# Kernel tuning notes

Measured on AMD Instinct MI355X. Metric: run time of the kernel, lower is better.

Reference implementation:

```python
import jax, jax.numpy as jnp
import numpy as np

LN_EPS = 1e-5

def _ln(x, g):
    # LayerNorm with no bias, matching torch (population variance)
    m = x.mean(-1, keepdims=True)
    v = x.var(-1, keepdims=True)
    return (x - m) / jnp.sqrt(v + LN_EPS) * g


def setup_inputs() -> dict:
    key = jax.random.key(0)
    ks = jax.random.split(key, 10)
    B, S, D, L, V = 4, 4096, 256, 6, 32000
    std = 0.02  # nn.init.normal_(std=0.02)
    tokens = jax.random.randint(ks[0], (B, S), 0, V)
    wte = jax.random.normal(ks[1], (V, D), jnp.float32) * std
    wpe = jax.random.normal(ks[2], (S + 1, D), jnp.float32) * std  # context_size+1 table
    g_e = jnp.ones((D,), jnp.float32)
    g_p = jnp.ones((D,), jnp.float32)
    g_out = jnp.ones((D,), jnp.float32)
    ff_w1 = jax.random.normal(ks[3], (D, 4 * D), jnp.float32) * std
    ff_w2 = jax.random.normal(ks[4], (4 * D, D), jnp.float32) * std
    Wq = jax.random.normal(ks[5], (L, D, D), jnp.float32) * std
    Wk = jax.random.normal(ks[6], (L, D, D), jnp.float32) * std
    Wv = jax.random.normal(ks[7], (L, D, D), jnp.float32) * std
    return {"tokens": tokens, "wte": wte, "wpe": wpe, "g_e": g_e, "g_p": g_p,
            "g_out": g_out, "ff_w1": ff_w1, "ff_w2": ff_w2,
            "Wq": Wq, "Wk": Wk, "Wv": Wv}


def reference(tokens, wte, wpe, g_e, g_p, g_out, ff_w1, ff_w2, Wq, Wk, Wv):
    B, S = tokens.shape
    D = wte.shape[1]
    L = Wq.shape[0]
    # embeddings + pre-LN (dropout = identity at eval)
    e = _ln(wte[tokens], g_e)                 # [B,S,D] token stream
    p = _ln(wpe[:S], g_p)                     # [S,D]   positional stream (batch-invariant)
    x = e + p[None]                           # [B,S,D]
    # covariate FF on positional stream (use_ppe=True): p = p + W2 @ gelu(W1 @ p)
    p = p + jax.nn.gelu(p @ ff_w1, approximate=False) @ ff_w2
    causal = jnp.tril(jnp.ones((S, S), bool))
    inv_sqrt_d = D ** -0.5
    for l in range(L):
        # use_ppe: Q=K from positional stream (batch-invariant), V from token embeds
        q = p @ Wq[l]                          # [S,D]
        k = p @ Wk[l]                          # [S,D]
        v = jnp.einsum('bsd,de->bse', e, Wv[l])  # [B,S,D]
        s = (q @ k.T) * inv_sqrt_d             # [S,S], shared across batch
        s = jnp.where(causal, s, -jnp.inf)
        a = jax.nn.softmax(s, axis=-1)
        x = x + jnp.einsum('st,btd->bsd', a, v)
    # targets=None path: last position only
    x = x[:, -1:, :]                           # [B,1,D]
    x = _ln(x, g_out)                          # use_ln_out
    logits = x @ _ln(wte, g_e).T               # tied output head through ln_e
    return logits                              # [B,1,V]
```

## Files before the change

kernel.cpp:

```cpp
#include <hip/hip_runtime.h>
#include <hip/hip_bf16.h>

#define LN_EPS 1e-5f

typedef __attribute__((ext_vector_type(8))) short s8v;
typedef __attribute__((ext_vector_type(4))) float f32x4;

__device__ __forceinline__ float wred_sum(float v) {
#pragma unroll
  for (int o = 32; o > 0; o >>= 1) v += __shfl_xor(v, o, 64);
  return v;
}
__device__ __forceinline__ float wred_max(float v) {
#pragma unroll
  for (int o = 32; o > 0; o >>= 1) v = fmaxf(v, __shfl_xor(v, o, 64));
  return v;
}
__device__ __forceinline__ float bsum256(float v, float* s4) {
  v = wred_sum(v);
  int lane = threadIdx.x & 63, w = threadIdx.x >> 6;
  __syncthreads();
  if (lane == 0) s4[w] = v;
  __syncthreads();
  return s4[0] + s4[1] + s4[2] + s4[3];
}
__device__ __forceinline__ float bmax256(float v, float* s4) {
  v = wred_max(v);
  int lane = threadIdx.x & 63, w = threadIdx.x >> 6;
  __syncthreads();
  if (lane == 0) s4[w] = v;
  __syncthreads();
  return fmaxf(fmaxf(s4[0], s4[1]), fmaxf(s4[2], s4[3]));
}
__device__ __forceinline__ float bf2f(unsigned short u) {
  union { unsigned int i; float f; } c;
  c.i = ((unsigned int)u) << 16;
  return c.f;
}
__device__ __forceinline__ unsigned short f2bf(float f) {
  __hip_bfloat16 h = (__hip_bfloat16)f;
  return *(unsigned short*)&h;
}
__device__ __forceinline__ float4 bf4(ushort4 u) {
  return (float4){bf2f(u.x), bf2f(u.y), bf2f(u.z), bf2f(u.w)};
}
__device__ __forceinline__ void async_cp16(const __hip_bfloat16* g, __hip_bfloat16* l) {
  __builtin_amdgcn_global_load_lds(
      (const __attribute__((address_space(1))) unsigned int*)g,
      (__attribute__((address_space(3))) unsigned int*)l, 16, 0, 0);
}

__global__ void prep_k(const float* __restrict__ wpe, const float* __restrict__ wte,
                       const int* __restrict__ tokens,
                       const float* __restrict__ g_p, const float* __restrict__ g_e,
                       const float* __restrict__ ff_w1,
                       unsigned short* __restrict__ p0b, unsigned short* __restrict__ e,
                       unsigned short* __restrict__ w1T, float* __restrict__ zeros) {
  __shared__ float lds[64][65];
  int bx = blockIdx.x, t = threadIdx.x;
  int w = t >> 6, lane = t & 63;

  if (bx < 5120) {
    int row;
    const float* g;
    const float4* src;
    if (bx < 1024) {
      row = bx * 4 + w;
      src = (const float4*)(wpe + (size_t)row * 256);
      g = g_p;
    } else {
      row = (bx - 1024) * 4 + w;
      int tok = tokens[row];
      src = (const float4*)(wte + (size_t)tok * 256);
      g = g_e;
    }
    float4 v = src[lane];
    float mean = wred_sum(v.x + v.y + v.z + v.w) * (1.f / 256.f);
    float4 d = {v.x - mean, v.y - mean, v.z - mean, v.w - mean};
    float var = wred_sum(d.x * d.x + d.y * d.y + d.z * d.z + d.w * d.w) * (1.f / 256.f);
    float r = rsqrtf(var + LN_EPS);
    float4 gv = ((const float4*)g)[lane];
    ushort4 ob = {f2bf(d.x * r * gv.x), f2bf(d.y * r * gv.y),
                  f2bf(d.z * r * gv.z), f2bf(d.w * r * gv.w)};
    if (bx < 1024) ((ushort4*)(p0b + (size_t)row * 256))[lane] = ob;
    else           ((ushort4*)(e   + (size_t)row * 256))[lane] = ob;
    return;
  }
  if (bx < 5184) {
    int i = bx - 5120;
    int bxx = i & 3, byy = i >> 2;
    int x = t & 63, y4 = t >> 6;
    int r0 = bxx * 64, c0 = byy * 64;
#pragma unroll
    for (int k = 0; k < 16; ++k) {
      int r = y4 * 16 + k;
      lds[r][x] = ff_w1[(size_t)(r0 + r) * 1024 + c0 + x];
    }
    __syncthreads();
#pragma unroll
    for (int k = 0; k < 16; ++k) {
      int a = y4 * 16 + k;
      w1T[(size_t)(c0 + a) * 256 + r0 + x] = f2bf(lds[x][a]);
    }
    return;
  }
  for (int i = t; i < 8976; i += 256) zeros[i] = 0.f;
}

__global__ __launch_bounds__(256, 4) void mfma_gemm(
    const __hip_bfloat16* __restrict__ A, const __hip_bfloat16* __restrict__ BT,
    __hip_bfloat16* __restrict__ Cout, int M, int N, int K, int mode) {
  __shared__ __hip_bfloat16 As[64 * 128];
  __shared__ __hip_bfloat16 Bs[64 * 128];
  const int t = threadIdx.x;
  const int lane = t & 63, wave = t >> 6;
  const int wr = wave >> 1, wc = wave & 1;
  const int fr = lane & 15, quad = lane >> 4;
  const int m0 = blockIdx.x * 64, n0 = blockIdx.y * 64;

  f32x4 acc[2][2];
#pragma unroll
  for (int i = 0; i < 2; ++i)
#pragma unroll
    for (int j = 0; j < 2; ++j) acc[i][j] = (f32x4){0.f, 0.f, 0.f, 0.f};

  for (int k0 = 0; k0 < K; k0 += 128) {
    __syncthreads();
#pragma unroll
    for (int j = 0; j < 4; ++j) {
      int ld = wave * 4 + j;
      int slot = ld * 64 + lane;
      int m = slot >> 4, c = slot & 15;
      const __hip_bfloat16* g = A + (size_t)(m0 + m) * K + k0 + ((c ^ (m & 15)) << 3);
      async_cp16(g, As + ld * 512);
    }
#pragma unroll
    for (int j = 0; j < 4; ++j) {
      int ld = wave * 4 + j;
      int slot = ld * 64 + lane;
      int n = slot >> 4, c = slot & 15;
      const __hip_bfloat16* g = BT + (size_t)(n0 + n) * K + k0 + ((c ^ (n & 15)) << 3);
      async_cp16(g, Bs + ld * 512);
    }
    __syncthreads();
#pragma unroll
    for (int h = 0; h < 4; ++h) {
      s8v af[2], bfv[2];
#pragma unroll
      for (int i = 0; i < 2; ++i) {
        int m = wr * 32 + i * 16 + fr;
        int ch = (h * 4 + quad) ^ (m & 15);
        af[i] = *(const s8v*)(As + m * 128 + ch * 8);
      }
#pragma unroll
      for (int j = 0; j < 2; ++j) {
        int n = wc * 32 + j * 16 + fr;
        int ch = (h * 4 + quad) ^ (n & 15);
        bfv[j] = *(const s8v*)(Bs + n * 128 + ch * 8);
      }
#pragma unroll
      for (int i = 0; i < 2; ++i)
#pragma unroll
        for (int j = 0; j < 2; ++j)
          acc[i][j] = __builtin_amdgcn_mfma_f32_16x16x32_bf16(af[i], bfv[j], acc[i][j], 0, 0, 0);
    }
  }

#pragma unroll
  for (int i = 0; i < 2; ++i) {
#pragma unroll
    for (int j = 0; j < 2; ++j) {
#pragma unroll
      for (int r = 0; r < 4; ++r) {
        int row = m0 + wr * 32 + i * 16 + quad * 4 + r;
        int col = n0 + wc * 32 + j * 16 + fr;
        float v = acc[i][j][r];
        if (mode == 1) v = 0.5f * v * (1.f + erff(v * 0.70710678118654752f));
        Cout[(size_t)row * N + col] = (__hip_bfloat16)v;
      }
    }
  }
}

__global__ void plast_k(const unsigned short* __restrict__ hB,
                        const unsigned short* __restrict__ p0b,
                        const float* __restrict__ W2, float* __restrict__ plast) {
  int c = blockIdx.x, t = threadIdx.x;
  float pa = (c == 0) ? bf2f(p0b[(size_t)4095 * 256 + t]) : 0.f;
#pragma unroll
  for (int i = 0; i < 16; ++i) {
    int k = c * 16 + i;
    pa += bf2f(hB[(size_t)4095 * 1024 + k]) * W2[(size_t)k * 256 + t];
  }
  atomicAdd(&plast[t], pa);
}

__global__ void q_k(const float* __restrict__ plast, const float* __restrict__ Wq,
                    float* __restrict__ qall) {
  int c = blockIdx.x, l = blockIdx.y, t = threadIdx.x;
  const float* W = Wq + (size_t)l * 65536;
  float pa = 0.f;
#pragma unroll
  for (int i = 0; i < 16; ++i) {
    int d = c * 16 + i;
    pa += plast[d] * W[d * 256 + t];
  }
  atomicAdd(&qall[l * 256 + t], pa);
}

__global__ void kv_k(const float* __restrict__ Wk, const float* __restrict__ qall,
                     float* __restrict__ kv) {
  int l = blockIdx.y;
  int w = threadIdx.x >> 6, lane = threadIdx.x & 63;
  int r = blockIdx.x * 4 + w;
  float4 wv = ((const float4*)(Wk + (size_t)l * 65536 + (size_t)r * 256))[lane];
  float4 qv = ((const float4*)(qall + l * 256))[lane];
  float dot = wred_sum(wv.x * qv.x + wv.y * qv.y + wv.z * qv.z + wv.w * qv.w);
  if (lane == 0) kv[l * 256 + r] = dot;
}

__global__ void w2kv_k(const float* __restrict__ W2, const float* __restrict__ kv,
                       float* __restrict__ w2kv) {
  int l = blockIdx.y;
  int w = threadIdx.x >> 6, lane = threadIdx.x & 63;
  int r = blockIdx.x * 4 + w;
  float4 wv = ((const float4*)(W2 + (size_t)r * 256))[lane];
  float4 qv = ((const float4*)(kv + l * 256))[lane];
  float dot = wred_sum(wv.x * qv.x + wv.y * qv.y + wv.z * qv.z + wv.w * qv.w);
  if (lane == 0) w2kv[l * 1024 + r] = dot;
}

__global__ __launch_bounds__(256) void sc_k(
    const unsigned short* __restrict__ p0b, const unsigned short* __restrict__ hB,
    const float* __restrict__ kv, const float* __restrict__ w2kv,
    float* __restrict__ sc) {
  __shared__ float skv[6 * 256];
  __shared__ float sw2[6 * 1024];
  int t = threadIdx.x;
  for (int i = t; i < 1536; i += 256) skv[i] = kv[i];
  for (int i = t; i < 6144; i += 256) sw2[i] = w2kv[i];
  __syncthreads();
  int wave = t >> 6, lane = t & 63;
#pragma unroll
  for (int rr = 0; rr < 2; ++rr) {
    int row = blockIdx.x * 8 + wave * 2 + rr;
    const ushort4* hrow = (const ushort4*)(hB + (size_t)row * 1024);
    float4 h0 = bf4(hrow[lane]);
    float4 h1 = bf4(hrow[64 + lane]);
    float4 h2 = bf4(hrow[128 + lane]);
    float4 h3 = bf4(hrow[192 + lane]);
    float4 p = bf4(((const ushort4*)(p0b + (size_t)row * 256))[lane]);
#pragma unroll
    for (int l = 0; l < 6; ++l) {
      float4 kf = ((const float4*)(skv + l * 256))[lane];
      float4 w0 = ((const float4*)(sw2 + l * 1024))[lane];
      float4 w1 = ((const float4*)(sw2 + l * 1024 + 256))[lane];
      float4 w2 = ((const float4*)(sw2 + l * 1024 + 512))[lane];
      float4 w3 = ((const float4*)(sw2 + l * 1024 + 768))[lane];
      float a = p.x * kf.x + p.y * kf.y + p.z * kf.z + p.w * kf.w;
      a += h0.x * w0.x + h0.y * w0.y + h0.z * w0.z + h0.w * w0.w;
      a += h1.x * w1.x + h1.y * w1.y + h1.z * w1.z + h1.w * w1.w;
      a += h2.x * w2.x + h2.y * w2.y + h2.z * w2.z + h2.w * w2.w;
      a += h3.x * w3.x + h3.y * w3.y + h3.z * w3.z + h3.w * w3.w;
      a = wred_sum(a);
      if (lane == 0) sc[(size_t)l * 4096 + row] = a * 0.0625f;
    }
  }
}

__global__ void ctx_sm_k(const unsigned short* __restrict__ e, const float* __restrict__ sc,
                         float* __restrict__ ctx) {
  int c = blockIdx.x, b = blockIdx.y, t = threadIdx.x;
  __shared__ float s4[4];
  __shared__ float wch[6][32];
  float wmax[6], winv[6];
#pragma unroll
  for (int l = 0; l < 6; ++l) {
    const float* scl = sc + (size_t)l * 4096;
    float lm = -1e30f;
    for (int i = t; i < 4096; i += 256) lm = fmaxf(lm, scl[i]);
    lm = bmax256(lm, s4);
    float ls = 0.f;
    for (int i = t; i < 4096; i += 256) ls += expf(scl[i] - lm);
    ls = bsum256(ls, s4);
    wmax[l] = lm; winv[l] = 1.f / ls;
  }
  if (t < 192) {
    int l = t >> 5, j = t & 31;
    wch[l][j] = expf(sc[(size_t)l * 4096 + c * 32 + j] - wmax[l]) * winv[l];
  }
  __syncthreads();
  const unsigned short* eb = e + ((size_t)b * 4096 + c * 32) * 256;
  float a[6] = {0.f, 0.f, 0.f, 0.f, 0.f, 0.f};
#pragma unroll 4
  for (int i = 0; i < 32; ++i) {
    float ev = bf2f(eb[(size_t)i * 256 + t]);
#pragma unroll
    for (int l = 0; l < 6; ++l) a[l] += wch[l][i] * ev;
  }
#pragma unroll
  for (int l = 0; l < 6; ++l) atomicAdd(&ctx[(l * 4 + b) * 256 + t], a[l]);
}

__global__ void proj_final_k(const float* __restrict__ ctx, const float* __restrict__ Wv,
                             float* __restrict__ xacc,
                             const unsigned short* __restrict__ e,
                             const unsigned short* __restrict__ p0b,
                             const float* __restrict__ gout, float* __restrict__ xln,
                             int* __restrict__ done) {
  int c = blockIdx.x, l = blockIdx.y, t = threadIdx.x;
  __shared__ float s4[4];
  __shared__ int tick;
  const float* W = Wv + (size_t)l * 65536;
  float pa[4] = {0.f, 0.f, 0.f, 0.f};
#pragma unroll
  for (int i = 0; i < 16; ++i) {
    int d = c * 16 + i;
    float wv = W[d * 256 + t];
#pragma unroll
    for (int b = 0; b < 4; ++b) pa[b] += ctx[(l * 4 + b) * 256 + d] * wv;
  }
#pragma unroll
  for (int b = 0; b < 4; ++b) atomicAdd(&xacc[b * 256 + t], pa[b]);
  __threadfence();
  if (t == 0) tick = atomicAdd(done, 1);
  __syncthreads();
  if (tick == 95) {
#pragma unroll
    for (int b = 0; b < 4; ++b) {
      float v = atomicAdd(&xacc[b * 256 + t], 0.f)
              + bf2f(e[((size_t)(b * 4096 + 4095)) * 256 + t])
              + bf2f(p0b[(size_t)4095 * 256 + t]);
      float mean = bsum256(v, s4) * (1.f / 256.f);
      float d = v - mean;
      float var = bsum256(d * d, s4) * (1.f / 256.f);
      xln[b * 256 + t] = d * rsqrtf(var + LN_EPS) * gout[t];
    }
  }
}

__global__ void logits_k(const float* __restrict__ wte, const float* __restrict__ ge,
                         const float* __restrict__ xln, float* __restrict__ out) {
  int wv = threadIdx.x >> 6, lane = threadIdx.x & 63;
  int v = blockIdx.x * 4 + wv;
  float4 x = ((const float4*)(wte + (size_t)v * 256))[lane];
  float mean = wred_sum(x.x + x.y + x.z + x.w) * (1.f / 256.f);
  float4 d = {x.x - mean, x.y - mean, x.z - mean, x.w - mean};
  float var = wred_sum(d.x * d.x + d.y * d.y + d.z * d.z + d.w * d.w) * (1.f / 256.f);
  float r = rsqrtf(var + LN_EPS);
  float4 gv = ((const float4*)ge)[lane];
  float4 ln = {d.x * r * gv.x, d.y * r * gv.y, d.z * r * gv.z, d.w * r * gv.w};
#pragma unroll
  for (int b = 0; b < 4; ++b) {
    float4 xv = ((const float4*)(xln + b * 256))[lane];
    float dot = wred_sum(ln.x * xv.x + ln.y * xv.y + ln.z * xv.z + ln.w * xv.w);
    if (lane == 0) out[b * 32000 + v] = dot;
  }
}

#define O_E     ((size_t)0)
#define O_P0B   ((size_t)2097152)
#define O_W1T   ((size_t)2621440)
#define O_HB    ((size_t)2752512)
#define O_CTX   ((size_t)4849664)
#define O_QALL  ((size_t)4855808)
#define O_XACC  ((size_t)4857344)
#define O_PLAST ((size_t)4858368)
#define O_DONE  ((size_t)4858624)
#define O_KV    ((size_t)4858640)
#define O_W2KV  ((size_t)4860176)
#define O_SC    ((size_t)4866320)
#define O_XLN   ((size_t)4890896)

extern "C" void kernel_launch(void* const* d_in, const int* in_sizes, int n_in,
                              void* d_out, int out_size, void* d_ws, size_t ws_size,
                              hipStream_t stream) {
  const int*   tokens = (const int*)d_in[0];
  const float* wte    = (const float*)d_in[1];
  const float* wpe    = (const float*)d_in[2];
  const float* g_e    = (const float*)d_in[3];
  const float* g_p    = (const float*)d_in[4];
  const float* g_out  = (const float*)d_in[5];
  const float* ff_w1  = (const float*)d_in[6];
  const float* ff_w2  = (const float*)d_in[7];
  const float* Wq     = (const float*)d_in[8];
  const float* Wk     = (const float*)d_in[9];
  const float* Wv     = (const float*)d_in[10];
  float* out = (float*)d_out;
  float* ws = (float*)d_ws;

  unsigned short* e   = (unsigned short*)(ws + O_E);
  unsigned short* p0b = (unsigned short*)(ws + O_P0B);
  unsigned short* w1T = (unsigned short*)(ws + O_W1T);
  unsigned short* hB  = (unsigned short*)(ws + O_HB);
  float* ctx   = ws + O_CTX;
  float* qall  = ws + O_QALL;
  float* xacc  = ws + O_XACC;
  float* plast = ws + O_PLAST;
  int*   done  = (int*)(ws + O_DONE);
  float* kv    = ws + O_KV;
  float* w2kv  = ws + O_W2KV;
  float* sc    = ws + O_SC;
  float* xln   = ws + O_XLN;

  prep_k<<<5185, 256, 0, stream>>>(wpe, wte, tokens, g_p, g_e, ff_w1,
                                   p0b, e, w1T, ctx);
  mfma_gemm<<<dim3(64, 16), 256, 0, stream>>>(
      (const __hip_bfloat16*)p0b, (const __hip_bfloat16*)w1T,
      (__hip_bfloat16*)hB, 4096, 1024, 256, 1);
  plast_k<<<64, 256, 0, stream>>>(hB, p0b, ff_w2, plast);
  q_k<<<dim3(16, 6), 256, 0, stream>>>(plast, Wq, qall);
  kv_k<<<dim3(64, 6), 256, 0, stream>>>(Wk, qall, kv);
  w2kv_k<<<dim3(256, 6), 256, 0, stream>>>(ff_w2, kv, w2kv);
  sc_k<<<512, 256, 0, stream>>>(p0b, hB, kv, w2kv, sc);
  ctx_sm_k<<<dim3(128, 4), 256, 0, stream>>>(e, sc, ctx);
  proj_final_k<<<dim3(16, 6), 256, 0, stream>>>(ctx, Wv, xacc, e, p0b, g_out, xln, done);
  logits_k<<<8000, 256, 0, stream>>>(wte, g_e, xln, out);
}
```

Baseline: 184.9 us.

## Compute softmax stats once in last sc_k block; shrink GEMM K-tile to 64

The softmax max and sum over the 6×4096 score rows were recomputed by all 512 ctx blocks. They are now computed once by the last block of sc_k, found with an atomic ticket counter, and stored in a small workspace buffer. ctx_k then only reads those values. Separately, the MFMA GEMM is templated and now uses a 64-wide K tile with an 8-chunk swizzle, which halves shared memory per block and may raise occupancy. The cost is a serial tail in sc_k while one block does the reduction, and a second done counter that needs a zeroed slot.

```diff
diff --git a/kernel.cpp b/kernel.cpp
--- a/kernel.cpp
+++ b/kernel.cpp
@@ -104,62 +104,64 @@
     }
     return;
   }
-  for (int i = t; i < 8976; i += 256) zeros[i] = 0.f;
-}
-
+  for (int i = t; i < 8992; i += 256) zeros[i] = 0.f;
+}
+
+template <int TM>
 __global__ __launch_bounds__(256, 4) void mfma_gemm(
     const __hip_bfloat16* __restrict__ A, const __hip_bfloat16* __restrict__ BT,
     __hip_bfloat16* __restrict__ Cout, int M, int N, int K, int mode) {
-  __shared__ __hip_bfloat16 As[64 * 128];
-  __shared__ __hip_bfloat16 Bs[64 * 128];
+  constexpr int BM = TM * 32;
+  __shared__ __hip_bfloat16 As[BM * 64];
+  __shared__ __hip_bfloat16 Bs[64 * 64];
   const int t = threadIdx.x;
   const int lane = t & 63, wave = t >> 6;
   const int wr = wave >> 1, wc = wave & 1;
   const int fr = lane & 15, quad = lane >> 4;
-  const int m0 = blockIdx.x * 64, n0 = blockIdx.y * 64;
-
-  f32x4 acc[2][2];
-#pragma unroll
-  for (int i = 0; i < 2; ++i)
+  const int m0 = blockIdx.x * BM, n0 = blockIdx.y * 64;
+
+  f32x4 acc[TM][2];
+#pragma unroll
+  for (int i = 0; i < TM; ++i)
 #pragma unroll
     for (int j = 0; j < 2; ++j) acc[i][j] = (f32x4){0.f, 0.f, 0.f, 0.f};
 
-  for (int k0 = 0; k0 < K; k0 += 128) {
+  for (int k0 = 0; k0 < K; k0 += 64) {
     __syncthreads();
 #pragma unroll
-    for (int j = 0; j < 4; ++j) {
-      int ld = wave * 4 + j;
+    for (int j = 0; j < TM; ++j) {
+      int ld = wave * TM + j;
       int slot = ld * 64 + lane;
-      int m = slot >> 4, c = slot & 15;
-      const __hip_bfloat16* g = A + (size_t)(m0 + m) * K + k0 + ((c ^ (m & 15)) << 3);
+      int m = slot >> 3, c = slot & 7;
+      const __hip_bfloat16* g = A + (size_t)(m0 + m) * K + k0 + ((c ^ (m & 7)) << 3);
       async_cp16(g, As + ld * 512);
     }
 #pragma unroll
-    for (int j = 0; j < 4; ++j) {
-      int ld = wave * 4 + j;
+    for (int j = 0; j < 2; ++j) {
+      int ld = wave * 2 + j;
       int slot = ld * 64 + lane;
-      int n = slot >> 4, c = slot & 15;
-      const __hip_bfloat16* g = BT + (size_t)(n0 + n) * K + k0 + ((c ^ (n & 15)) << 3);
+      int n = slot >> 3, c = slot & 7;
+      const __hip_bfloat16* g = BT + (size_t)(n0 + n) * K + k0 + ((c ^ (n & 7)) << 3);
       async_cp16(g, Bs + ld * 512);
     }
     __syncthreads();
 #pragma unroll
-    for (int h = 0; h < 4; ++h) {
-      s8v af[2], bfv[2];
-#pragma unroll
-      for (int i = 0; i < 2; ++i) {
-        int m = wr * 32 + i * 16 + fr;
-        int ch = (h * 4 + quad) ^ (m & 15);
-        af[i] = *(const s8v*)(As + m * 128 + ch * 8);
+    for (int h = 0; h < 2; ++h) {
+      s8v af[TM], bfv[2];
+#pragma unroll
+      for (int i = 0; i < TM; ++i) {
+        int m = wr * TM * 16 + i * 16 + fr;
+        int ch = (h * 4 + quad) ^ (m & 7);
+        af[i] = *(const s8v*)(As + m * 64 + ch * 8);
       }
 #pragma unroll
       for (int j = 0; j < 2; ++j) {
         int n = wc * 32 + j * 16 + fr;
-        int ch = (h * 4 + quad) ^ (n & 15);
-        bfv[j] = *(const s8v*)(Bs + n * 128 + ch * 8);
+        int ch = (h * 4 + quad) ^ (n & 7);
+        bfv[j] = *(const s8v*)(Bs + n * 64 + ch * 8);
       }
 #pragma unroll
-      for (int i = 0; i < 2; ++i)
+      for (int i = 0; i < TM; ++i)
 #pragma unroll
         for (int j = 0; j < 2; ++j)
           acc[i][j] = __builtin_amdgcn_mfma_f32_16x16x32_bf16(af[i], bfv[j], acc[i][j], 0, 0, 0);
@@ -167,12 +169,12 @@
   }
 
 #pragma unroll
-  for (int i = 0; i < 2; ++i) {
+  for (int i = 0; i < TM; ++i) {
 #pragma unroll
     for (int j = 0; j < 2; ++j) {
 #pragma unroll
       for (int r = 0; r < 4; ++r) {
-        int row = m0 + wr * 32 + i * 16 + quad * 4 + r;
+        int row = m0 + wr * TM * 16 + i * 16 + quad * 4 + r;
         int col = n0 + wc * 32 + j * 16 + fr;
         float v = acc[i][j][r];
         if (mode == 1) v = 0.5f * v * (1.f + erff(v * 0.70710678118654752f));
@@ -233,9 +235,11 @@
 __global__ __launch_bounds__(256) void sc_k(
     const unsigned short* __restrict__ p0b, const unsigned short* __restrict__ hB,
     const float* __restrict__ kv, const float* __restrict__ w2kv,
-    float* __restrict__ sc) {
+    float* __restrict__ sc, float* __restrict__ smx, int* __restrict__ done) {
   __shared__ float skv[6 * 256];
   __shared__ float sw2[6 * 1024];
+  __shared__ float s4[4];
+  __shared__ int tick;
   int t = threadIdx.x;
   for (int i = t; i < 1536; i += 256) skv[i] = kv[i];
   for (int i = t; i < 6144; i += 256) sw2[i] = w2kv[i];
@@ -266,28 +270,32 @@
       if (lane == 0) sc[(size_t)l * 4096 + row] = a * 0.0625f;
     }
   }
-}
-
-__global__ void ctx_sm_k(const unsigned short* __restrict__ e, const float* __restrict__ sc,
-                         float* __restrict__ ctx) {
+  __threadfence();
+  if (t == 0) tick = atomicAdd(done, 1);
+  __syncthreads();
+  if (tick == 511) {
+    __threadfence();
+#pragma unroll
+    for (int l = 0; l < 6; ++l) {
+      const float* scl = sc + (size_t)l * 4096;
+      float lm = -1e30f;
+      for (int i = t; i < 4096; i += 256) lm = fmaxf(lm, scl[i]);
+      lm = bmax256(lm, s4);
+      float ls = 0.f;
+      for (int i = t; i < 4096; i += 256) ls += expf(scl[i] - lm);
+      ls = bsum256(ls, s4);
+      if (t == 0) { smx[l] = lm; smx[6 + l] = 1.f / ls; }
+    }
+  }
+}
+
+__global__ void ctx_k(const unsigned short* __restrict__ e, const float* __restrict__ sc,
+                      const float* __restrict__ smx, float* __restrict__ ctx) {
   int c = blockIdx.x, b = blockIdx.y, t = threadIdx.x;
-  __shared__ float s4[4];
   __shared__ float wch[6][32];
-  float wmax[6], winv[6];
-#pragma unroll
-  for (int l = 0; l < 6; ++l) {
-    const float* scl = sc + (size_t)l * 4096;
-    float lm = -1e30f;
-    for (int i = t; i < 4096; i += 256) lm = fmaxf(lm, scl[i]);
-    lm = bmax256(lm, s4);
-    float ls = 0.f;
-    for (int i = t; i < 4096; i += 256) ls += expf(scl[i] - lm);
-    ls = bsum256(ls, s4);
-    wmax[l] = lm; winv[l] = 1.f / ls;
-  }
   if (t < 192) {
     int l = t >> 5, j = t & 31;
-    wch[l][j] = expf(sc[(size_t)l * 4096 + c * 32 + j] - wmax[l]) * winv[l];
+    wch[l][j] = expf(sc[(size_t)l * 4096 + c * 32 + j] - smx[l]) * smx[6 + l];
   }
   __syncthreads();
   const unsigned short* eb = e + ((size_t)b * 4096 + c * 32) * 256;
@@ -366,11 +374,12 @@
 #define O_QALL  ((size_t)4855808)
 #define O_XACC  ((size_t)4857344)
 #define O_PLAST ((size_t)4858368)
-#define O_DONE  ((size_t)4858624)
-#define O_KV    ((size_t)4858640)
-#define O_W2KV  ((size_t)4860176)
-#define O_SC    ((size_t)4866320)
-#define O_XLN   ((size_t)4890896)
+#define O_SMX   ((size_t)4858624)
+#define O_DONE  ((size_t)4858640)
+#define O_KV    ((size_t)4858656)
+#define O_W2KV  ((size_t)4860192)
+#define O_SC    ((size_t)4866336)
+#define O_XLN   ((size_t)4890912)
 
 extern "C" void kernel_launch(void* const* d_in, const int* in_sizes, int n_in,
                               void* d_out, int out_size, void* d_ws, size_t ws_size,
@@ -397,6 +406,7 @@
   float* qall  = ws + O_QALL;
   float* xacc  = ws + O_XACC;
   float* plast = ws + O_PLAST;
+  float* smx   = ws + O_SMX;
   int*   done  = (int*)(ws + O_DONE);
   float* kv    = ws + O_KV;
   float* w2kv  = ws + O_W2KV;
@@ -405,15 +415,15 @@
 
   prep_k<<<5185, 256, 0, stream>>>(wpe, wte, tokens, g_p, g_e, ff_w1,
                                    p0b, e, w1T, ctx);
-  mfma_gemm<<<dim3(64, 16), 256, 0, stream>>>(
+  mfma_gemm<2><<<dim3(64, 16), 256, 0, stream>>>(
       (const __hip_bfloat16*)p0b, (const __hip_bfloat16*)w1T,
       (__hip_bfloat16*)hB, 4096, 1024, 256, 1);
   plast_k<<<64, 256, 0, stream>>>(hB, p0b, ff_w2, plast);
   q_k<<<dim3(16, 6), 256, 0, stream>>>(plast, Wq, qall);
   kv_k<<<dim3(64, 6), 256, 0, stream>>>(Wk, qall, kv);
   w2kv_k<<<dim3(256, 6), 256, 0, stream>>>(ff_w2, kv, w2kv);
-  sc_k<<<512, 256, 0, stream>>>(p0b, hB, kv, w2kv, sc);
-  ctx_sm_k<<<dim3(128, 4), 256, 0, stream>>>(e, sc, ctx);
-  proj_final_k<<<dim3(16, 6), 256, 0, stream>>>(ctx, Wv, xacc, e, p0b, g_out, xln, done);
+  sc_k<<<512, 256, 0, stream>>>(p0b, hB, kv, w2kv, sc, smx, done);
+  ctx_k<<<dim3(128, 4), 256, 0, stream>>>(e, sc, smx, ctx);
+  proj_final_k<<<dim3(16, 6), 256, 0, stream>>>(ctx, Wv, xacc, e, p0b, g_out, xln, done + 1);
   logits_k<<<8000, 256, 0, stream>>>(wte, g_e, xln, out);
 }
```

Result: slower. 223.7 us (+21.0%).
